# Kernel tuning notes

Measured on AMD Instinct MI355X. Metric: run time of the kernel, lower is better.

## Reference

```python
import jax, jax.numpy as jnp
import numpy as np

NUM_EMBEDDINGS = 1024
EMBEDDING_DIM = 256
COMMITMENT_COST = 0.25


def setup_inputs() -> dict:
    key = jax.random.key(0)
    k1, k2 = jax.random.split(key)
    inputs = jax.random.normal(k1, (32, EMBEDDING_DIM, 32, 32), dtype=jnp.float32)
    # codebook init matches torch: uniform(-1/K, 1/K)
    weight = jax.random.uniform(
        k2, (NUM_EMBEDDINGS, EMBEDDING_DIM), dtype=jnp.float32,
        minval=-1.0 / NUM_EMBEDDINGS, maxval=1.0 / NUM_EMBEDDINGS)
    return {"inputs": inputs, "weight": weight}


def reference(inputs, weight):
    # inputs: [B, C, H, W] with C == EMBEDDING_DIM; weight: [K, D]
    x = jnp.transpose(inputs, (0, 2, 3, 1))            # [B, H, W, D]
    input_shape = x.shape
    flat = x.reshape(-1, EMBEDDING_DIM)                # [N, D]

    distances = (jnp.sum(flat * flat, axis=1, keepdims=True)
                 + jnp.sum(weight * weight, axis=1)
                 - 2.0 * (flat @ weight.T))
    encoding_indices = jnp.argmin(distances, axis=1)   # [N]
    encodings = jax.nn.one_hot(encoding_indices, NUM_EMBEDDINGS, dtype=jnp.float32)  # [N, K]

    # one_hot @ weight == gather; use gather for efficiency (same values)
    quantized = weight[encoding_indices].reshape(input_shape)  # [B, H, W, D]

    e_latent_loss = jnp.mean((jax.lax.stop_gradient(quantized) - x) ** 2)
    q_latent_loss = jnp.mean((quantized - jax.lax.stop_gradient(x)) ** 2)
    loss = q_latent_loss + COMMITMENT_COST * e_latent_loss

    # straight-through estimator
    quantized_st = x + jax.lax.stop_gradient(quantized - x)

    avg_probs = jnp.mean(encodings, axis=0)            # [K]
    perplexity = jnp.exp(-jnp.sum(avg_probs * jnp.log(avg_probs + 1e-10)))

    return (loss,
            jnp.transpose(quantized_st, (0, 3, 1, 2)),  # back to [B, C, H, W]
            perplexity,
            encodings)
```

## Files before the change

kernel.cpp:

```cpp
#include <hip/hip_runtime.h>
#include <hip/hip_bf16.h>

#define HWDIM 1024
#define DDIM 256
#define KCODES 1024
#define NROWS 32768
#define BSTRIDE (DDIM * HWDIM)
#define GUARD 1.5e-4f

typedef __attribute__((ext_vector_type(8))) short short8;
typedef __attribute__((ext_vector_type(4))) float f32x4;
typedef unsigned long long ull;


__device__ __forceinline__ unsigned short f2bf(float v) {
  __hip_bfloat16 b = __float2bfloat16(v);
  return *reinterpret_cast<unsigned short*>(&b);
}
__device__ __forceinline__ float bf2f(unsigned short u) {
  __hip_bfloat16 b;
  *reinterpret_cast<unsigned short*>(&b) = u;
  return __bfloat162float(b);
}
__device__ __forceinline__ ull pk(float d, int k) {
  unsigned ub = __float_as_uint(d);
  ub = (ub & 0x80000000u) ? ~ub : (ub | 0x80000000u);
  return ((ull)ub << 32) | (unsigned)k;
}
__device__ __forceinline__ float keyq(ull key) {
  unsigned ub = (unsigned)(key >> 32);
  unsigned orig = (ub & 0x80000000u) ? (ub & 0x7FFFFFFFu) : ~ub;
  return __uint_as_float(orig);
}
__device__ __forceinline__ float keyq32(unsigned ub) {
  unsigned orig = (ub & 0x80000000u) ? (ub & 0x7FFFFFFFu) : ~ub;
  return __uint_as_float(orig);
}

__device__ __forceinline__ float pair128_sq(const float* p, int stride) {
  float a[8];
#pragma unroll
  for (int j = 0; j < 8; ++j) { float v = p[j * stride]; a[j] = __fmul_rn(v, v); }
  for (int i = 8; i < 128; i += 8) {
#pragma unroll
    for (int j = 0; j < 8; ++j) {
      float v = p[(i + j) * stride];
      a[j] = __fadd_rn(a[j], __fmul_rn(v, v));
    }
  }
  float s01 = __fadd_rn(a[0], a[1]), s23 = __fadd_rn(a[2], a[3]);
  float s45 = __fadd_rn(a[4], a[5]), s67 = __fadd_rn(a[6], a[7]);
  return __fadd_rn(__fadd_rn(s01, s23), __fadd_rn(s45, s67));
}

__global__ __launch_bounds__(256) void k_prep(
    const float* __restrict__ w, float* __restrict__ wT, float* __restrict__ ss,
    int* __restrict__ hist, double* __restrict__ loss,
    int* __restrict__ wcount, int* __restrict__ pcount,
    unsigned short* __restrict__ wh8, unsigned short* __restrict__ wl8) {
  __shared__ float tile[64][65];
  const int t = threadIdx.x;
  int g = blockIdx.x * 256 + t;
  {
    int k = g >> 5, oct = g & 31;
    const float* p = w + k * DDIM + oct * 8;
    short8 hv, lv;
#pragma unroll
    for (int j = 0; j < 8; ++j) {
      float v = p[j];
      unsigned short h = f2bf(v);
      unsigned short l = f2bf(__fsub_rn(v, bf2f(h)));
      hv[j] = (short)h; lv[j] = (short)l;
    }
    *(short8*)&wh8[oct * 8192 + k * 8] = hv;
    *(short8*)&wl8[oct * 8192 + k * 8] = lv;
  }
  if (g < KCODES) {
    hist[g] = 0;
    const float* p = w + g * DDIM;
    ss[g] = __fadd_rn(pair128_sq(p, 1), pair128_sq(p + 128, 1));
  }
  if (g == 0) { *loss = 0.0; *wcount = 0; *pcount = 0; }
  if (blockIdx.x < 64) {
    const int k0 = (blockIdx.x & 15) * 64, d0 = (blockIdx.x >> 4) * 64;
    const int c = t & 63, r = t >> 6;
#pragma unroll
    for (int m = 0; m < 16; ++m)
      tile[r + m * 4][c] = w[(k0 + r + m * 4) * DDIM + d0 + c];
    __syncthreads();
#pragma unroll
    for (int m = 0; m < 16; ++m)
      wT[(size_t)(d0 + r + m * 4) * KCODES + k0 + c] = tile[c][r + m * 4];
  }
}

__global__ __launch_bounds__(512, 2) void k_argmfma(
    const float* __restrict__ in,
    const unsigned short* __restrict__ wh8, const unsigned short* __restrict__ wl8,
    const float* __restrict__ ss, unsigned* __restrict__ kkarr,
    int* __restrict__ wlist, int* __restrict__ wcount,
    int* __restrict__ plist, int* __restrict__ pcount) {
  __shared__ __align__(16) char smem[131072];
  __shared__ __align__(16) float ss_l[1024];
  __shared__ ull best1[128], best2[128];
  __shared__ unsigned best3[128];

  const int t = threadIdx.x;
  const int n0 = blockIdx.x * 128;
  const int b = n0 >> 10, hw0 = n0 & 1023;

  const int wv = t >> 6, ln = t & 63;
  const int rw = wv * 16;
  const int l15 = ln & 15, quad = ln >> 4;

  unsigned short* Ah = (unsigned short*)smem;
  unsigned short* Al = (unsigned short*)(smem + 65536);

  {
    const int hw = t & 127, dg = t >> 7;
    const float* xp = in + b * BSTRIDE + hw0 + hw;
#pragma unroll
    for (int dd = 0; dd < 64; dd += 2) {
      int d = dg * 64 + dd;
      float f0 = __builtin_nontemporal_load(&xp[d * HWDIM]);
      float f1 = __builtin_nontemporal_load(&xp[(d + 1) * HWDIM]);
      unsigned short h0 = f2bf(f0);
      unsigned short l0 = f2bf(__fsub_rn(f0, bf2f(h0)));
      unsigned short h1 = f2bf(f1);
      unsigned short l1 = f2bf(__fsub_rn(f1, bf2f(h1)));
      int base = ((d >> 3) * 128 + hw) * 8 + (d & 7);
      *(unsigned*)&Ah[base] = (unsigned)h0 | ((unsigned)h1 << 16);
      *(unsigned*)&Al[base] = (unsigned)l0 | ((unsigned)l1 << 16);
    }
  }
  *(float2*)&ss_l[t * 2] = *(const float2*)&ss[t * 2];
  if (t < 128) { best1[t] = ~0ull; best2[t] = ~0ull; best3[t] = 0xFFFFFFFFu; }
  __syncthreads();

  short8 afh[8], afl[8];
  {
    const int row = rw + l15;
#pragma unroll
    for (int ki = 0; ki < 8; ++ki) {
      int obase = ki * 4 + quad;
      afh[ki] = *(const short8*)&Ah[(obase * 128 + row) * 8];
      afl[ki] = *(const short8*)&Al[(obase * 128 + row) * 8];
    }
  }
  short8 s0h[4], s0l[4];
#pragma unroll
  for (int j = 0; j < 4; ++j) {
    int u = j * 512 + t;
    int ob = u >> 6, c = u & 63;
    s0h[j] = *(const short8*)&wh8[ob * 8192 + c * 8];
    s0l[j] = *(const short8*)&wl8[ob * 8192 + c * 8];
  }
  __syncthreads();

  {
    unsigned short* Bh0 = (unsigned short*)smem;
    unsigned short* Bl0 = (unsigned short*)(smem + 32768);
#pragma unroll
    for (int j = 0; j < 4; ++j) {
      int u = j * 512 + t;
      *(short8*)&Bh0[u * 8] = s0h[j];
      *(short8*)&Bl0[u * 8] = s0l[j];
    }
  }
  __syncthreads();

  ull rb1[4], rb2[4];
  unsigned rb3[4];
#pragma unroll
  for (int i = 0; i < 4; ++i) { rb1[i] = ~0ull; rb2[i] = ~0ull; rb3[i] = 0xFFFFFFFFu; }

  int cur = 0;
  for (int s = 0; s < 16; ++s) {
    const int cb = s * 64;
    short8 sh_[4], sl_[4];
    if (s < 15) {
      const int cb1 = cb + 64;
#pragma unroll
      for (int j = 0; j < 4; ++j) {
        int u = j * 512 + t;
        int ob = u >> 6, c = u & 63;
        sh_[j] = *(const short8*)&wh8[ob * 8192 + (cb1 + c) * 8];
        sl_[j] = *(const short8*)&wl8[ob * 8192 + (cb1 + c) * 8];
      }
    }

    const unsigned short* Bh = (const unsigned short*)(smem + cur * 65536);
    const unsigned short* Bl = (const unsigned short*)(smem + cur * 65536 + 32768);
    f32x4 acc[4];
#pragma unroll
    for (int ct = 0; ct < 4; ++ct) acc[ct] = (f32x4){0.f, 0.f, 0.f, 0.f};

#pragma unroll
    for (int ki = 0; ki < 8; ++ki) {
      const int obase = ki * 4 + quad;
      short8 bh[4], bl[4];
#pragma unroll
      for (int ct = 0; ct < 4; ++ct) {
        int uo = (obase * 64 + ct * 16 + l15) * 8;
        bh[ct] = *(const short8*)&Bh[uo];
        bl[ct] = *(const short8*)&Bl[uo];
      }
#pragma unroll
      for (int ct = 0; ct < 4; ++ct) {
        acc[ct] = __builtin_amdgcn_mfma_f32_16x16x32_bf16(afh[ki], bh[ct], acc[ct], 0, 0, 0);
        acc[ct] = __builtin_amdgcn_mfma_f32_16x16x32_bf16(afh[ki], bl[ct], acc[ct], 0, 0, 0);
        acc[ct] = __builtin_amdgcn_mfma_f32_16x16x32_bf16(afl[ki], bh[ct], acc[ct], 0, 0, 0);
      }
    }

    float sv[4];
#pragma unroll
    for (int ct = 0; ct < 4; ++ct) sv[ct] = ss_l[cb + ct * 16 + l15];
#pragma unroll
    for (int reg = 0; reg < 4; ++reg) {
      ull b1 = rb1[reg], b2 = rb2[reg];
      unsigned b3 = rb3[reg];
#pragma unroll
      for (int ct = 0; ct < 4; ++ct) {
        float q = fmaf(-2.f, acc[ct][reg], sv[ct]);
        ull key = pk(q, cb + ct * 16 + l15);
        unsigned k32 = (unsigned)(key >> 32);
        if (key < b1)      { b3 = (unsigned)(b2 >> 32); b2 = b1; b1 = key; }
        else if (key < b2) { b3 = (unsigned)(b2 >> 32); b2 = key; }
        else if (k32 < b3) { b3 = k32; }
      }
      rb1[reg] = b1; rb2[reg] = b2; rb3[reg] = b3;
    }

    if (s < 15) {
      unsigned short* BhN = (unsigned short*)(smem + (cur ^ 1) * 65536);
      unsigned short* BlN = (unsigned short*)(smem + (cur ^ 1) * 65536 + 32768);
#pragma unroll
      for (int j = 0; j < 4; ++j) {
        int u = j * 512 + t;
        *(short8*)&BhN[u * 8] = sh_[j];
        *(short8*)&BlN[u * 8] = sl_[j];
      }
    }
    __syncthreads();
    cur ^= 1;
  }

#pragma unroll
  for (int reg = 0; reg < 4; ++reg)
    atomicMin(&best1[rw + quad * 4 + reg], rb1[reg]);
  __syncthreads();
#pragma unroll
  for (int reg = 0; reg < 4; ++reg) {
    int row = rw + quad * 4 + reg;
    ull sub = (rb1[reg] == best1[row]) ? rb2[reg] : rb1[reg];
    atomicMin(&best2[row], sub);
  }
  __syncthreads();
#pragma unroll
  for (int reg = 0; reg < 4; ++reg) {
    int row = rw + quad * 4 + reg;
    ull b1 = best1[row], b2 = best2[row];
    unsigned c = (rb1[reg] != b1 && rb1[reg] != b2) ? (unsigned)(rb1[reg] >> 32)
               : ((rb2[reg] != b1 && rb2[reg] != b2) ? (unsigned)(rb2[reg] >> 32)
                                                     : rb3[reg]);
    atomicMin(&best3[row], c);
  }
  __syncthreads();
  if (t < 128) {
    ull k1 = best1[t];
    kkarr[n0 + t] = (unsigned)(k1 & 0xFFFFFFFFull);
    float q1 = keyq(k1);
    if (!(keyq(best2[t]) - q1 > GUARD)) {
      if (keyq32(best3[t]) - q1 > GUARD) {
        int p = atomicAdd(pcount, 1);
        plist[p] = (n0 + t) | ((int)(best2[t] & 0xFFFFFFFFull) << 16);
      } else {
        int p = atomicAdd(wcount, 1);
        wlist[p] = n0 + t;
      }
    }
  }
}

__global__ __launch_bounds__(256) void k_fallback(
    const float* __restrict__ in, const float* __restrict__ w,
    const float* __restrict__ wT, const float* __restrict__ ss,
    const int* __restrict__ wlist, const int* __restrict__ wcount,
    const int* __restrict__ plist, const int* __restrict__ pcount,
    unsigned* __restrict__ kkarr) {
  __shared__ float xrow[256];
  __shared__ float rsh;
  __shared__ ull bmin;
  __shared__ ull pkeys[2];
  const int t = threadIdx.x;

  const int pc = *pcount;
  for (int i = blockIdx.x; i < pc; i += gridDim.x) {
    const int pe = plist[i];
    const int n = pe & 0xFFFF;
    const unsigned k2 = ((unsigned)pe) >> 16;
    const unsigned k1 = kkarr[n];
    const int b = n >> 10, hw = n & 1023;
    xrow[t] = in[b * BSTRIDE + t * HWDIM + hw];
    __syncthreads();
    if (t == 0) rsh = __fadd_rn(pair128_sq(xrow, 1), pair128_sq(xrow + 128, 1));
    __syncthreads();
    if (t < 2) {
      unsigned k = t ? k2 : k1;
      const float* wr = w + (size_t)k * DDIM;
      float m = 0.f;
      for (int d = 0; d < 256; ++d) m = fmaf(xrow[d], wr[d], m);
      float dist = fmaf(-2.f, m, __fadd_rn(rsh, ss[k]));
      pkeys[t] = pk(dist, (int)k);
    }
    __syncthreads();
    if (t == 0) {
      ull kmin = pkeys[0] < pkeys[1] ? pkeys[0] : pkeys[1];
      kkarr[n] = (unsigned)(kmin & 0xFFFFFFFFull);
    }
    __syncthreads();
  }

  const int cnt = *wcount;
  for (int i = blockIdx.x; i < cnt; i += gridDim.x) {
    const int n = wlist[i];
    const int b = n >> 10, hw = n & 1023;
    xrow[t] = in[b * BSTRIDE + t * HWDIM + hw];
    if (t == 0) bmin = ~0ull;
    __syncthreads();
    if (t == 0) rsh = __fadd_rn(pair128_sq(xrow, 1), pair128_sq(xrow + 128, 1));
    __syncthreads();
    float m[4] = {0.f, 0.f, 0.f, 0.f};
    for (int d = 0; d < 256; ++d) {
      float xv = xrow[d];
      const float* wd = wT + (size_t)d * KCODES + t;
      m[0] = fmaf(xv, wd[0], m[0]);
      m[1] = fmaf(xv, wd[256], m[1]);
      m[2] = fmaf(xv, wd[512], m[2]);
      m[3] = fmaf(xv, wd[768], m[3]);
    }
    ull lb = ~0ull;
#pragma unroll
    for (int j = 0; j < 4; ++j) {
      int k = t + j * 256;
      float dist = fmaf(-2.f, m[j], __fadd_rn(rsh, ss[k]));
      ull key = pk(dist, k);
      if (key < lb) lb = key;
    }
    atomicMin(&bmin, lb);
    __syncthreads();
    if (t == 0) kkarr[n] = (unsigned)(bmin & 0xFFFFFFFFull);
    __syncthreads();
  }
}

__global__ __launch_bounds__(256) void k_quantenc(
    const float* __restrict__ in, const float* __restrict__ w,
    const unsigned* __restrict__ kkarr, int* __restrict__ hist,
    float* __restrict__ enc, float* __restrict__ outq, double* __restrict__ loss) {
  __shared__ float wrow[64][65];
  __shared__ unsigned kk[64];
  __shared__ double red[256];

  const int t = threadIdx.x;
  const int q = blockIdx.x & 3;
  const int n0 = (blockIdx.x >> 2) * 64;
  const int dc = q * 64;
  const int c0 = q * 256;
  const int b = n0 >> 10, hw0 = n0 & 1023;

  if (t < 64) kk[t] = kkarr[n0 + t];
  __syncthreads();

  if (q == 0 && t < 64) atomicAdd(&hist[kk[t]], 1);

#pragma unroll 4
  for (int m = 0; m < 32; ++m) {
    int u = m * 256 + t;
    int r = u >> 7, c2 = u & 127;
    int cbase = c0 + c2 * 2;
    unsigned kr = kk[r];
    float2 v;
    v.x = (cbase == (int)kr) ? 1.0f : 0.0f;
    v.y = (cbase + 1 == (int)kr) ? 1.0f : 0.0f;
    *(float2*)&enc[(size_t)(n0 + r) * 1024 + cbase] = v;
  }

#pragma unroll
  for (int m = 0; m < 16; ++m) {
    int u = t + m * 256;
    int r = u >> 6, dd = u & 63;
    wrow[r][dd] = w[kk[r] * DDIM + dc + dd];
  }
  __syncthreads();

  const float* inb = in + b * BSTRIDE + hw0;
  float* outb = outq + b * BSTRIDE + hw0;
  const int hwl = t & 63, dl = t >> 6;
  double lsum = 0.0;
#pragma unroll
  for (int dd = 0; dd < 64; dd += 4) {
    int d = dc + dd + dl;
    float x = inb[d * HWDIM + hwl];
    float wv = wrow[hwl][dd + dl];
    float diff = __fsub_rn(wv, x);
    outb[d * HWDIM + hwl] = __fadd_rn(x, diff);
    lsum += (double)diff * (double)diff;
  }
  red[t] = lsum;
  __syncthreads();
  for (int s = 128; s > 0; s >>= 1) {
    if (t < s) red[t] += red[t + s];
    __syncthreads();
  }
  if (t == 0) atomicAdd(loss, red[0]);
}

__global__ void k_final(const int* __restrict__ hist, const double* __restrict__ loss,
                        float* __restrict__ out) {
  __shared__ double red[256];
  int t = threadIdx.x;
  double s = 0.0;
  for (int i = t; i < KCODES; i += 256) {
    double p = (double)hist[i] * (1.0 / 32768.0);
    s += p * log(p + 1e-10);
  }
  red[t] = s;
  __syncthreads();
  for (int st = 128; st > 0; st >>= 1) {
    if (t < st) red[t] += red[t + st];
    __syncthreads();
  }
  if (t == 0) {
    out[8388609] = (float)exp(-red[0]);
    double m = *loss / 8388608.0;
    out[0] = (float)(1.25 * m);
  }
}

extern "C" void kernel_launch(void* const* d_in, const int* in_sizes, int n_in,
                              void* d_out, int out_size, void* d_ws, size_t ws_size,
                              hipStream_t stream) {
  const float* in = (const float*)d_in[0];
  const float* w  = (const float*)d_in[1];
  float* out = (float*)d_out;

  char* wsb = (char*)d_ws;
  float*    wT     = (float*)   (wsb + 0);
  float*    ssp    = (float*)   (wsb + 1048576);
  unsigned* kkarr  = (unsigned*)(wsb + 1052672);
  int*      wlist  = (int*)     (wsb + 1183744);
  int*      hist   = (int*)     (wsb + 1314816);
  int*      plist  = (int*)     (wsb + 1318912);
  double*   loss   = (double*)  (wsb + 1449984);
  int*      wcount = (int*)     (wsb + 1449992);
  int*      pcount = (int*)     (wsb + 1449996);

  char* ob = (char*)d_out + 33554448;
  unsigned short* wh8 = (unsigned short*)(ob + 0);
  unsigned short* wl8 = (unsigned short*)(ob + 524288);
  float* encp = out + 8388610;

  k_prep<<<dim3(128), dim3(256), 0, stream>>>(w, wT, ssp, hist, loss, wcount, pcount, wh8, wl8);
  k_argmfma<<<dim3(256), dim3(512), 0, stream>>>(in, wh8, wl8, ssp, kkarr,
                                                 wlist, wcount, plist, pcount);
  k_fallback<<<dim3(1024), dim3(256), 0, stream>>>(in, w, wT, ssp, wlist, wcount,
                                                   plist, pcount, kkarr);
  k_quantenc<<<dim3(2048), dim3(256), 0, stream>>>(in, w, kkarr, hist, encp,
                                                   out + 1, loss);
  k_final<<<dim3(1), dim3(256), 0, stream>>>(hist, loss, out);
}
```

Before: 314.9 us.

## Retile argmin MFMA per wave to 32x32 and use nontemporal output stores

After: 329.6 us. 1.05x slower.

```diff
diff --git a/kernel.cpp b/kernel.cpp
--- a/kernel.cpp
+++ b/kernel.cpp
@@ -110,7 +110,8 @@
   const int b = n0 >> 10, hw0 = n0 & 1023;
 
   const int wv = t >> 6, ln = t & 63;
-  const int rw = wv * 16;
+  const int rowbase = (wv >> 1) * 32;
+  const int ch = wv & 1;
   const int l15 = ln & 15, quad = ln >> 4;
 
   unsigned short* Ah = (unsigned short*)smem;
@@ -137,14 +138,15 @@
   if (t < 128) { best1[t] = ~0ull; best2[t] = ~0ull; best3[t] = 0xFFFFFFFFu; }
   __syncthreads();
 
-  short8 afh[8], afl[8];
-  {
-    const int row = rw + l15;
+  short8 afh[2][8], afl[2][8];
+#pragma unroll
+  for (int rt = 0; rt < 2; ++rt) {
+    const int row = rowbase + rt * 16 + l15;
 #pragma unroll
     for (int ki = 0; ki < 8; ++ki) {
       int obase = ki * 4 + quad;
-      afh[ki] = *(const short8*)&Ah[(obase * 128 + row) * 8];
-      afl[ki] = *(const short8*)&Al[(obase * 128 + row) * 8];
+      afh[rt][ki] = *(const short8*)&Ah[(obase * 128 + row) * 8];
+      afl[rt][ki] = *(const short8*)&Al[(obase * 128 + row) * 8];
     }
   }
   short8 s0h[4], s0l[4];
@@ -169,10 +171,10 @@
   }
   __syncthreads();
 
-  ull rb1[4], rb2[4];
-  unsigned rb3[4];
-#pragma unroll
-  for (int i = 0; i < 4; ++i) { rb1[i] = ~0ull; rb2[i] = ~0ull; rb3[i] = 0xFFFFFFFFu; }
+  ull rb1[8], rb2[8];
+  unsigned rb3[8];
+#pragma unroll
+  for (int i = 0; i < 8; ++i) { rb1[i] = ~0ull; rb2[i] = ~0ull; rb3[i] = 0xFFFFFFFFu; }
 
   int cur = 0;
   for (int s = 0; s < 16; ++s) {
@@ -191,46 +193,53 @@
 
     const unsigned short* Bh = (const unsigned short*)(smem + cur * 65536);
     const unsigned short* Bl = (const unsigned short*)(smem + cur * 65536 + 32768);
-    f32x4 acc[4];
-#pragma unroll
-    for (int ct = 0; ct < 4; ++ct) acc[ct] = (f32x4){0.f, 0.f, 0.f, 0.f};
+    f32x4 acc[2][2];
+#pragma unroll
+    for (int rt = 0; rt < 2; ++rt)
+#pragma unroll
+      for (int ct = 0; ct < 2; ++ct) acc[rt][ct] = (f32x4){0.f, 0.f, 0.f, 0.f};
 
 #pragma unroll
     for (int ki = 0; ki < 8; ++ki) {
       const int obase = ki * 4 + quad;
-      short8 bh[4], bl[4];
-#pragma unroll
-      for (int ct = 0; ct < 4; ++ct) {
-        int uo = (obase * 64 + ct * 16 + l15) * 8;
+      short8 bh[2], bl[2];
+#pragma unroll
+      for (int ct = 0; ct < 2; ++ct) {
+        int uo = (obase * 64 + ch * 32 + ct * 16 + l15) * 8;
         bh[ct] = *(const short8*)&Bh[uo];
         bl[ct] = *(const short8*)&Bl[uo];
       }
 #pragma unroll
-      for (int ct = 0; ct < 4; ++ct) {
-        acc[ct] = __builtin_amdgcn_mfma_f32_16x16x32_bf16(afh[ki], bh[ct], acc[ct], 0, 0, 0);
-        acc[ct] = __builtin_amdgcn_mfma_f32_16x16x32_bf16(afh[ki], bl[ct], acc[ct], 0, 0, 0);
-        acc[ct] = __builtin_amdgcn_mfma_f32_16x16x32_bf16(afl[ki], bh[ct], acc[ct], 0, 0, 0);
+      for (int rt = 0; rt < 2; ++rt)
+#pragma unroll
+        for (int ct = 0; ct < 2; ++ct) {
+          acc[rt][ct] = __builtin_amdgcn_mfma_f32_16x16x32_bf16(afh[rt][ki], bh[ct], acc[rt][ct], 0, 0, 0);
+          acc[rt][ct] = __builtin_amdgcn_mfma_f32_16x16x32_bf16(afh[rt][ki], bl[ct], acc[rt][ct], 0, 0, 0);
+          acc[rt][ct] = __builtin_amdgcn_mfma_f32_16x16x32_bf16(afl[rt][ki], bh[ct], acc[rt][ct], 0, 0, 0);
+        }
+    }
+
+    float sv[2];
+#pragma unroll
+    for (int ct = 0; ct < 2; ++ct) sv[ct] = ss_l[cb + ch * 32 + ct * 16 + l15];
+#pragma unroll
+    for (int rt = 0; rt < 2; ++rt)
+#pragma unroll
+      for (int reg = 0; reg < 4; ++reg) {
+        int idx = rt * 4 + reg;
+        ull b1 = rb1[idx], b2 = rb2[idx];
+        unsigned b3 = rb3[idx];
+#pragma unroll
+        for (int ct = 0; ct < 2; ++ct) {
+          float q = fmaf(-2.f, acc[rt][ct][reg], sv[ct]);
+          ull key = pk(q, cb + ch * 32 + ct * 16 + l15);
+          unsigned k32 = (unsigned)(key >> 32);
+          if (key < b1)      { b3 = (unsigned)(b2 >> 32); b2 = b1; b1 = key; }
+          else if (key < b2) { b3 = (unsigned)(b2 >> 32); b2 = key; }
+          else if (k32 < b3) { b3 = k32; }
+        }
+        rb1[idx] = b1; rb2[idx] = b2; rb3[idx] = b3;
       }
-    }
-
-    float sv[4];
-#pragma unroll
-    for (int ct = 0; ct < 4; ++ct) sv[ct] = ss_l[cb + ct * 16 + l15];
-#pragma unroll
-    for (int reg = 0; reg < 4; ++reg) {
-      ull b1 = rb1[reg], b2 = rb2[reg];
-      unsigned b3 = rb3[reg];
-#pragma unroll
-      for (int ct = 0; ct < 4; ++ct) {
-        float q = fmaf(-2.f, acc[ct][reg], sv[ct]);
-        ull key = pk(q, cb + ct * 16 + l15);
-        unsigned k32 = (unsigned)(key >> 32);
-        if (key < b1)      { b3 = (unsigned)(b2 >> 32); b2 = b1; b1 = key; }
-        else if (key < b2) { b3 = (unsigned)(b2 >> 32); b2 = key; }
-        else if (k32 < b3) { b3 = k32; }
-      }
-      rb1[reg] = b1; rb2[reg] = b2; rb3[reg] = b3;
-    }
 
     if (s < 15) {
       unsigned short* BhN = (unsigned short*)(smem + (cur ^ 1) * 65536);
@@ -247,25 +256,33 @@
   }
 
 #pragma unroll
-  for (int reg = 0; reg < 4; ++reg)
-    atomicMin(&best1[rw + quad * 4 + reg], rb1[reg]);
-  __syncthreads();
-#pragma unroll
-  for (int reg = 0; reg < 4; ++reg) {
-    int row = rw + quad * 4 + reg;
-    ull sub = (rb1[reg] == best1[row]) ? rb2[reg] : rb1[reg];
-    atomicMin(&best2[row], sub);
-  }
-  __syncthreads();
-#pragma unroll
-  for (int reg = 0; reg < 4; ++reg) {
-    int row = rw + quad * 4 + reg;
-    ull b1 = best1[row], b2 = best2[row];
-    unsigned c = (rb1[reg] != b1 && rb1[reg] != b2) ? (unsigned)(rb1[reg] >> 32)
-               : ((rb2[reg] != b1 && rb2[reg] != b2) ? (unsigned)(rb2[reg] >> 32)
-                                                     : rb3[reg]);
-    atomicMin(&best3[row], c);
-  }
+  for (int rt = 0; rt < 2; ++rt)
+#pragma unroll
+    for (int reg = 0; reg < 4; ++reg)
+      atomicMin(&best1[rowbase + rt * 16 + quad * 4 + reg], rb1[rt * 4 + reg]);
+  __syncthreads();
+#pragma unroll
+  for (int rt = 0; rt < 2; ++rt)
+#pragma unroll
+    for (int reg = 0; reg < 4; ++reg) {
+      int row = rowbase + rt * 16 + quad * 4 + reg;
+      int idx = rt * 4 + reg;
+      ull sub = (rb1[idx] == best1[row]) ? rb2[idx] : rb1[idx];
+      atomicMin(&best2[row], sub);
+    }
+  __syncthreads();
+#pragma unroll
+  for (int rt = 0; rt < 2; ++rt)
+#pragma unroll
+    for (int reg = 0; reg < 4; ++reg) {
+      int row = rowbase + rt * 16 + quad * 4 + reg;
+      int idx = rt * 4 + reg;
+      ull b1 = best1[row], b2 = best2[row];
+      unsigned c = (rb1[idx] != b1 && rb1[idx] != b2) ? (unsigned)(rb1[idx] >> 32)
+                 : ((rb2[idx] != b1 && rb2[idx] != b2) ? (unsigned)(rb2[idx] >> 32)
+                                                       : rb3[idx]);
+      atomicMin(&best3[row], c);
+    }
   __syncthreads();
   if (t < 128) {
     ull k1 = best1[t];
@@ -381,10 +398,10 @@
     int r = u >> 7, c2 = u & 127;
     int cbase = c0 + c2 * 2;
     unsigned kr = kk[r];
-    float2 v;
-    v.x = (cbase == (int)kr) ? 1.0f : 0.0f;
-    v.y = (cbase + 1 == (int)kr) ? 1.0f : 0.0f;
-    *(float2*)&enc[(size_t)(n0 + r) * 1024 + cbase] = v;
+    union { float2 f; double d; } v;
+    v.f.x = (cbase == (int)kr) ? 1.0f : 0.0f;
+    v.f.y = (cbase + 1 == (int)kr) ? 1.0f : 0.0f;
+    __builtin_nontemporal_store(v.d, (double*)&enc[(size_t)(n0 + r) * 1024 + cbase]);
   }
 
 #pragma unroll
@@ -402,10 +419,10 @@
 #pragma unroll
   for (int dd = 0; dd < 64; dd += 4) {
     int d = dc + dd + dl;
-    float x = inb[d * HWDIM + hwl];
+    float x = __builtin_nontemporal_load(&inb[d * HWDIM + hwl]);
     float wv = wrow[hwl][dd + dl];
     float diff = __fsub_rn(wv, x);
-    outb[d * HWDIM + hwl] = __fadd_rn(x, diff);
+    __builtin_nontemporal_store(__fadd_rn(x, diff), &outb[d * HWDIM + hwl]);
     lsum += (double)diff * (double)diff;
   }
   red[t] = lsum;
```
